# Performance work log

Hardware: AMD Instinct MI355X
Metric: run time of the kernel (lower is better)

Reference implementation:

```python
import jax, jax.numpy as jnp
import numpy as np

N, E = 50000, 800000
D_IN, D_HID, D_OUT = 128, 128, 64


def sage_conv(x, src, dst, w_l, w_r, b, n_nodes):
    # PyG SAGEConv (aggr='mean', root_weight=True):
    #   out = lin_l(mean_{j in N(i)} x_j) + lin_r(x_i)
    msg_sum = jax.ops.segment_sum(x[src], dst, num_segments=n_nodes)  # [N, d]
    cnt = jax.ops.segment_sum(jnp.ones((src.shape[0],), x.dtype), dst,
                              num_segments=n_nodes)                   # [N]
    mean = msg_sum / jnp.maximum(cnt, 1.0)[:, None]
    return mean @ w_l.T + x @ w_r.T + b


def prelu(x, a):
    return jnp.maximum(x, 0) + a * jnp.minimum(x, 0)


def setup_inputs() -> dict:
    key = jax.random.key(0)
    ks = jax.random.split(key, 12)
    def lin(k, o, i):
        s = 1.0 / np.sqrt(i)
        return jax.random.uniform(k, (o, i), jnp.float32, -s, s)
    x = jax.random.normal(ks[0], (N, D_IN), jnp.float32)
    edge_index = jax.random.randint(ks[1], (2, E), 0, N, jnp.int64)
    return {
        "x": x,
        "edge_index": edge_index,
        "w1l": lin(ks[2], D_HID, D_IN),  "w1r": lin(ks[3], D_HID, D_IN),
        "b1": jnp.zeros((D_HID,), jnp.float32),
        "w2l": lin(ks[4], D_HID, D_HID), "w2r": lin(ks[5], D_HID, D_HID),
        "b2": jnp.zeros((D_HID,), jnp.float32),
        "w3l": lin(ks[6], D_OUT, D_HID), "w3r": lin(ks[7], D_OUT, D_HID),
        "b3": jnp.zeros((D_OUT,), jnp.float32),
        "a": jnp.array(0.25, jnp.float32),  # shared PReLU slope
        "wp": lin(ks[8], 1, D_OUT),
        "bp": jnp.zeros((1,), jnp.float32),
    }


def reference(x, edge_index, w1l, w1r, b1, w2l, w2r, b2, w3l, w3r, b3, a, wp, bp):
    src, dst = edge_index[0], edge_index[1]
    n = x.shape[0]
    h = prelu(sage_conv(x, src, dst, w1l, w1r, b1, n), a)
    h = prelu(sage_conv(h, src, dst, w2l, w2r, b2, n), a)
    h = sage_conv(h, src, dst, w3l, w3r, b3, n)          # [N, D_OUT]
    level = (h @ wp.T + bp).squeeze(-1)                  # [N]
    return level
```

## Files before the change

kernel.cpp:

```cpp
#include <hip/hip_runtime.h>
#include <cstdint>
#include <cstddef>

typedef float f32x4 __attribute__((ext_vector_type(4)));
typedef short short8 __attribute__((ext_vector_type(8)));
typedef __bf16 bf16x8 __attribute__((ext_vector_type(8)));

__device__ __forceinline__ void mfma_bf16(f32x4& d, short8 a, short8 b){
  d = __builtin_amdgcn_mfma_f32_16x16x32_bf16(
        __builtin_bit_cast(bf16x8, a), __builtin_bit_cast(bf16x8, b), d, 0, 0, 0);
}

__device__ __forceinline__ unsigned short bf16_rn(float f){
  unsigned u = __float_as_uint(f);
  unsigned r = (u + 0x7FFF + ((u >> 16) & 1)) >> 16;
  return (unsigned short)r;
}

__device__ __forceinline__ int blockScan256Excl(int v, int* wsum){
  const int lane = threadIdx.x & 63, wv = threadIdx.x >> 6;
  int x = v;
  #pragma unroll
  for (int off = 1; off < 64; off <<= 1){
    int y = __shfl_up(x, off);
    if (lane >= off) x += y;
  }
  if (lane == 63) wsum[wv] = x;
  __syncthreads();
  int woff = 0;
  #pragma unroll
  for (int w = 0; w < 4; ++w) woff += (w < wv) ? wsum[w] : 0;
  return woff + x - v;
}

__global__ __launch_bounds__(256) void k_bcount(const int* __restrict__ dst, int E, int nb, int ntiles,
                                                int* __restrict__ blk_hist){
  __shared__ int h[256];
  const int tile = blockIdx.x;
  h[threadIdx.x] = 0;
  __syncthreads();
  const int base = tile * 2048;
  const int end = min(base + 2048, E);
  for (int i = base + threadIdx.x; i < end; i += 256)
    atomicAdd(&h[dst[i] >> 8], 1);
  __syncthreads();
  const int b = threadIdx.x;
  if (b < nb) blk_hist[(size_t)b * ntiles + tile] = h[b];
}

__global__ __launch_bounds__(256) void k_bscan(int* __restrict__ blk_hist, int nb, int ntiles,
                                               int* __restrict__ tot){
  __shared__ int wsum[4];
  __shared__ int carry;
  const int b = blockIdx.x;
  int* row = blk_hist + (size_t)b * ntiles;
  if (threadIdx.x == 0) carry = 0;
  __syncthreads();
  const int lane = threadIdx.x & 63, wv = threadIdx.x >> 6;
  for (int base = 0; base < ntiles; base += 256){
    const int i = base + threadIdx.x;
    const int v = (i < ntiles) ? row[i] : 0;
    int x = v;
    #pragma unroll
    for (int off = 1; off < 64; off <<= 1){
      int y = __shfl_up(x, off);
      if (lane >= off) x += y;
    }
    if (lane == 63) wsum[wv] = x;
    __syncthreads();
    int woff = 0;
    #pragma unroll
    for (int w = 0; w < 4; ++w) woff += (w < wv) ? wsum[w] : 0;
    const int incl = carry + woff + x;
    if (i < ntiles) row[i] = incl - v;
    __syncthreads();
    if (threadIdx.x == 255) carry = incl;
    __syncthreads();
  }
  if (threadIdx.x == 0) tot[b] = carry;
}

__global__ __launch_bounds__(256) void k_btot(const int* __restrict__ tot, int nb,
                                              int* __restrict__ bucket_base){
  __shared__ int wsum[4];
  const int t = threadIdx.x;
  const int v = (t < nb) ? tot[t] : 0;
  const int e = blockScan256Excl(v, wsum);
  if (t <= nb) bucket_base[t] = e;
}

__global__ __launch_bounds__(256) void k_bscat(const int* __restrict__ src, const int* __restrict__ dst,
                                               int E, int nb, int ntiles,
                                               const int* __restrict__ blk_off,
                                               const int* __restrict__ bucket_base,
                                               unsigned* __restrict__ ebuf){
  __shared__ int cnt[256];
  __shared__ int lofs[256];
  __shared__ int gbase[256];
  __shared__ unsigned sorted[2048];
  __shared__ unsigned char sb[2048];
  __shared__ int wsum[4];
  const int tile = blockIdx.x;
  cnt[threadIdx.x] = 0;
  __syncthreads();
  const int base = tile * 2048;
  const int end = min(base + 2048, E);
  const int m = end - base;

  int rank_[8]; int b_[8]; unsigned v_[8];
  #pragma unroll
  for (int k = 0; k < 8; ++k){
    const int j = threadIdx.x + k * 256;
    if (base + j < end){
      const int d = dst[base + j];
      const int s = src[base + j];
      const int b = d >> 8;
      b_[k] = b;
      v_[k] = ((unsigned)(d & 255) << 16) | (unsigned)s;
      rank_[k] = atomicAdd(&cnt[b], 1);
    } else b_[k] = -1;
  }
  __syncthreads();
  const int ex = blockScan256Excl(cnt[threadIdx.x], wsum);
  lofs[threadIdx.x] = ex;
  if (threadIdx.x < nb)
    gbase[threadIdx.x] = bucket_base[threadIdx.x] + blk_off[(size_t)threadIdx.x * ntiles + tile];
  __syncthreads();
  #pragma unroll
  for (int k = 0; k < 8; ++k){
    if (b_[k] >= 0){
      const int p = lofs[b_[k]] + rank_[k];
      sorted[p] = v_[k];
      sb[p] = (unsigned char)b_[k];
    }
  }
  __syncthreads();
  for (int j = threadIdx.x; j < m; j += 256){
    const int b = sb[j];
    ebuf[gbase[b] + (j - lofs[b])] = sorted[j];
  }
}

__global__ __launch_bounds__(256) void k_csrfin(const unsigned* __restrict__ ebuf,
                                                const int* __restrict__ bucket_base,
                                                int n, int E, int nb,
                                                int* __restrict__ row_ptr,
                                                float* __restrict__ inv,
                                                unsigned short* __restrict__ csr){
  __shared__ int hist[256], excl[256], cursor[256];
  __shared__ int wsum[4];
  __shared__ unsigned vals[8192];
  __shared__ unsigned short sorted[8192];
  const int b = blockIdx.x;
  const int ebase = bucket_base[b];
  const int ecnt = bucket_base[b + 1] - ebase;
  const int t = threadIdx.x;
  hist[t] = 0;
  __syncthreads();
  for (int j = t; j < ecnt; j += 256){
    const unsigned v = ebuf[ebase + j];
    vals[j] = v;
    atomicAdd(&hist[v >> 16], 1);
  }
  __syncthreads();
  const int ex = blockScan256Excl(hist[t], wsum);
  excl[t] = ex;
  cursor[t] = ex;
  const int node = b * 256 + t;
  if (node < n){
    row_ptr[node] = ebase + ex;
    const int c = hist[t];
    inv[node] = 1.0f / (float)(c > 0 ? c : 1);
  }
  if (b == nb - 1 && t == 0) row_ptr[n] = E;
  __syncthreads();
  for (int j = t; j < ecnt; j += 256){
    const unsigned v = vals[j];
    const int pos = atomicAdd(&cursor[v >> 16], 1);
    sorted[pos] = (unsigned short)(v & 0xFFFFu);
  }
  __syncthreads();
  for (int j = t; j < ecnt; j += 256)
    csr[ebase + j] = sorted[j];
}

__global__ __launch_bounds__(256) void k_cvt(const float* __restrict__ in,
                                             unsigned short* __restrict__ out, int total){
  const int i = (blockIdx.x * 256 + threadIdx.x) * 4;
  if (i >= total) return;
  const float4 v = *(const float4*)&in[i];
  ushort2 a, b;
  a.x = bf16_rn(v.x); a.y = bf16_rn(v.y);
  b.x = bf16_rn(v.z); b.y = bf16_rn(v.w);
  *(ushort2*)&out[i] = a;
  *(ushort2*)&out[i + 2] = b;
}

__global__ __launch_bounds__(256) void k_aggb(const unsigned short* __restrict__ featb,
                                              const unsigned short* __restrict__ csr,
                                              const int* __restrict__ row_ptr,
                                              const float* __restrict__ inv_cnt,
                                              unsigned short* __restrict__ outb, int n){
  const int lane = threadIdx.x & 63;
  const int node = (blockIdx.x * blockDim.x + threadIdx.x) >> 6;
  if (node >= n) return;
  const int beg = row_ptr[node];
  const int end = row_ptr[node + 1];
  const unsigned* __restrict__ fb = (const unsigned*)featb;

  float ax0=0.f, ay0=0.f, ax1=0.f, ay1=0.f, ax2=0.f, ay2=0.f, ax3=0.f, ay3=0.f;
  float ax4=0.f, ay4=0.f, ax5=0.f, ay5=0.f, ax6=0.f, ay6=0.f, ax7=0.f, ay7=0.f;

  int j = beg;
  for (; j + 8 <= end; j += 8){
    const int s0 = csr[j+0], s1 = csr[j+1], s2 = csr[j+2], s3 = csr[j+3];
    const int s4 = csr[j+4], s5 = csr[j+5], s6 = csr[j+6], s7 = csr[j+7];
    const unsigned u0 = fb[(size_t)s0 * 64 + lane];
    const unsigned u1 = fb[(size_t)s1 * 64 + lane];
    const unsigned u2 = fb[(size_t)s2 * 64 + lane];
    const unsigned u3 = fb[(size_t)s3 * 64 + lane];
    const unsigned u4 = fb[(size_t)s4 * 64 + lane];
    const unsigned u5 = fb[(size_t)s5 * 64 + lane];
    const unsigned u6 = fb[(size_t)s6 * 64 + lane];
    const unsigned u7 = fb[(size_t)s7 * 64 + lane];
    ax0 += __uint_as_float(u0 << 16); ay0 += __uint_as_float(u0 & 0xFFFF0000u);
    ax1 += __uint_as_float(u1 << 16); ay1 += __uint_as_float(u1 & 0xFFFF0000u);
    ax2 += __uint_as_float(u2 << 16); ay2 += __uint_as_float(u2 & 0xFFFF0000u);
    ax3 += __uint_as_float(u3 << 16); ay3 += __uint_as_float(u3 & 0xFFFF0000u);
    ax4 += __uint_as_float(u4 << 16); ay4 += __uint_as_float(u4 & 0xFFFF0000u);
    ax5 += __uint_as_float(u5 << 16); ay5 += __uint_as_float(u5 & 0xFFFF0000u);
    ax6 += __uint_as_float(u6 << 16); ay6 += __uint_as_float(u6 & 0xFFFF0000u);
    ax7 += __uint_as_float(u7 << 16); ay7 += __uint_as_float(u7 & 0xFFFF0000u);
  }
  if (j + 4 <= end){
    const int s0 = csr[j+0], s1 = csr[j+1], s2 = csr[j+2], s3 = csr[j+3];
    const unsigned u0 = fb[(size_t)s0 * 64 + lane];
    const unsigned u1 = fb[(size_t)s1 * 64 + lane];
    const unsigned u2 = fb[(size_t)s2 * 64 + lane];
    const unsigned u3 = fb[(size_t)s3 * 64 + lane];
    ax0 += __uint_as_float(u0 << 16); ay0 += __uint_as_float(u0 & 0xFFFF0000u);
    ax1 += __uint_as_float(u1 << 16); ay1 += __uint_as_float(u1 & 0xFFFF0000u);
    ax2 += __uint_as_float(u2 << 16); ay2 += __uint_as_float(u2 & 0xFFFF0000u);
    ax3 += __uint_as_float(u3 << 16); ay3 += __uint_as_float(u3 & 0xFFFF0000u);
    j += 4;
  }
  for (; j < end; ++j){
    const int s = csr[j];
    const unsigned u = fb[(size_t)s * 64 + lane];
    ax4 += __uint_as_float(u << 16); ay4 += __uint_as_float(u & 0xFFFF0000u);
  }

  const float ic = inv_cnt[node];
  const float ox = (((ax0 + ax1) + (ax2 + ax3)) + ((ax4 + ax5) + (ax6 + ax7))) * ic;
  const float oy = (((ay0 + ay1) + (ay2 + ay3)) + ((ay4 + ay5) + (ay6 + ay7))) * ic;
  const unsigned packed = (unsigned)bf16_rn(ox) | ((unsigned)bf16_rn(oy) << 16);
  ((unsigned*)outb)[(size_t)node * 64 + lane] = packed;
}

__global__ void k_wcs(const float* __restrict__ wl, const float* __restrict__ wr,
                      short* __restrict__ bfr){
  int id = blockIdx.x * 256 + threadIdx.x;
  if (id >= 128 * 256) return;
  int c = id >> 8, k = id & 255;
  float w = (k < 128) ? wl[c * 128 + k] : wr[c * 128 + (k - 128)];
  unsigned short h = bf16_rn(w);
  float hf = __uint_as_float((unsigned)h << 16);
  unsigned short l = bf16_rn(w - hf);
  const int nt = c >> 4, mrow = c & 15;
  const int ks = k >> 5, kgrp = (k >> 3) & 3, j = k & 7;
  const int lane = kgrp * 16 + mrow;
  const size_t fbase = (size_t)((ks * 8 + nt) * 2) * 512 + lane * 8 + j;
  bfr[fbase] = (short)h;
  bfr[fbase + 512] = (short)l;
}

__global__ __launch_bounds__(256) void k_gemm_mfma(const unsigned short* __restrict__ A0b,
                                                   const unsigned short* __restrict__ A1b,
                                                   const short* __restrict__ bfr,
                                                   const float* __restrict__ bias,
                                                   const float* __restrict__ alpha_p,
                                                   float* __restrict__ outf,
                                                   unsigned short* __restrict__ outb16,
                                                   int n){
  __shared__ short aT[2][64 * 128];
  const int t = threadIdx.x;
  const int lane = t & 63;
  const int wv = t >> 6;
  const int nodeBase = blockIdx.x * 64;

  #pragma unroll
  for (int tab = 0; tab < 2; ++tab){
    const unsigned short* __restrict__ src = tab ? A1b : A0b;
    #pragma unroll
    for (int it = 0; it < 4; ++it){
      const int chunk = it * 256 + t;
      const int row = chunk >> 4;
      const int slot = chunk & 15;
      int gr = nodeBase + row; if (gr > n - 1) gr = n - 1;
      const uint4 v = *(const uint4*)&src[(size_t)gr * 128 + slot * 8];
      const int sslot = slot ^ (row & 7);
      *(uint4*)((char*)&aT[tab][0] + row * 256 + sslot * 16) = v;
    }
  }
  __syncthreads();

  const short8* __restrict__ Bf = (const short8*)bfr;
  const int mrow = lane & 15;
  const int kgrp = lane >> 4;
  const int arow = wv * 16 + mrow;

  f32x4 acc[8];
  #pragma unroll
  for (int i = 0; i < 8; ++i) acc[i] = (f32x4){0.f, 0.f, 0.f, 0.f};

  #pragma unroll
  for (int ks = 0; ks < 8; ++ks){
    const int tab = ks >> 2;
    const int slot_r = (ks & 3) * 4 + kgrp;
    const short8 aF = *(const short8*)((const char*)&aT[tab][0] + arow * 256 + (slot_r ^ (arow & 7)) * 16);

    short8 bh[8], bl[8];
    const int fb = ks * 16;
    #pragma unroll
    for (int nt = 0; nt < 8; ++nt){
      bh[nt] = Bf[(size_t)(fb + nt * 2 + 0) * 64 + lane];
      bl[nt] = Bf[(size_t)(fb + nt * 2 + 1) * 64 + lane];
    }
    #pragma unroll
    for (int nt = 0; nt < 8; ++nt){
      mfma_bf16(acc[nt], aF, bh[nt]);
      mfma_bf16(acc[nt], aF, bl[nt]);
    }
  }

  const float alpha = *alpha_p;
  const int nodeQ = nodeBase + wv * 16 + kgrp * 4;
  #pragma unroll
  for (int nt = 0; nt < 8; ++nt){
    const int col = nt * 16 + mrow;
    const float bv = bias[col];
    #pragma unroll
    for (int j = 0; j < 4; ++j){
      const int onode = nodeQ + j;
      if (onode < n){
        float v = acc[nt][j] + bv;
        v = fmaxf(v, 0.f) + alpha * fminf(v, 0.f);
        if (outf)   outf[(size_t)onode * 128 + col] = v;
        if (outb16) outb16[(size_t)onode * 128 + col] = bf16_rn(v);
      }
    }
  }
}

__global__ void k_u(const float* __restrict__ w3l, const float* __restrict__ w3r,
                    const float* __restrict__ b3, const float* __restrict__ wp,
                    const float* __restrict__ bp, float* __restrict__ u){
  int k = threadIdx.x;
  float sl = 0.f, sr = 0.f;
  for (int o = 0; o < 64; ++o){
    float w = wp[o];
    sl = fmaf(w, w3l[o * 128 + k], sl);
    sr = fmaf(w, w3r[o * 128 + k], sr);
  }
  u[k] = sl; u[128 + k] = sr;
  if (k == 0){
    float c = bp[0];
    for (int o = 0; o < 64; ++o) c = fmaf(wp[o], b3[o], c);
    u[256] = c;
  }
}

__global__ __launch_bounds__(256) void k_dot(const float* __restrict__ h,
                                             const float* __restrict__ u,
                                             float* __restrict__ s,
                                             float* __restrict__ partial, int n){
  const int lane = threadIdx.x & 63;
  const int i = blockIdx.x * 4 + (threadIdx.x >> 6);
  if (i >= n) return;
  const float2 hv  = *(const float2*)&h[(size_t)i * 128 + lane * 2];
  const float2 ulv = *(const float2*)&u[lane * 2];
  const float2 urv = *(const float2*)&u[128 + lane * 2];
  float sv = hv.x * ulv.x + hv.y * ulv.y;
  float tv = hv.x * urv.x + hv.y * urv.y;
  #pragma unroll
  for (int off = 32; off > 0; off >>= 1){
    sv += __shfl_down(sv, off);
    tv += __shfl_down(tv, off);
  }
  if (lane == 0){ s[i] = sv; partial[i] = tv + u[256]; }
}

__global__ __launch_bounds__(256) void k_final(const float* __restrict__ s, const float* __restrict__ partial,
                        const unsigned short* __restrict__ csr, const int* __restrict__ row_ptr,
                        const float* __restrict__ inv_cnt, float* __restrict__ out, int n){
  const int t = blockIdx.x * blockDim.x + threadIdx.x;
  const int node = t >> 2;
  const int sub = t & 3;
  if (node >= n) return;
  const int b = row_ptr[node], e = row_ptr[node + 1];
  float a0 = 0.f, a1 = 0.f;
  int j = b + sub;
  for (; j + 4 < e; j += 8){
    a0 += s[csr[j]];
    a1 += s[csr[j + 4]];
  }
  if (j < e) a0 += s[csr[j]];
  float acc = a0 + a1;
  acc += __shfl_down(acc, 1);
  acc += __shfl_down(acc, 2);
  if (sub == 0) out[node] = acc * inv_cnt[node] + partial[node];
}

extern "C" void kernel_launch(void* const* d_in, const int* in_sizes, int n_in,
                              void* d_out, int out_size, void* d_ws, size_t ws_size,
                              hipStream_t stream){
  const float* x   = (const float*)d_in[0];
  const int*   ei  = (const int*)d_in[1];
  const float* w1l = (const float*)d_in[2];
  const float* w1r = (const float*)d_in[3];
  const float* b1  = (const float*)d_in[4];
  const float* w2l = (const float*)d_in[5];
  const float* w2r = (const float*)d_in[6];
  const float* b2  = (const float*)d_in[7];
  const float* w3l = (const float*)d_in[8];
  const float* w3r = (const float*)d_in[9];
  const float* b3  = (const float*)d_in[10];
  const float* ap  = (const float*)d_in[11];
  const float* wp  = (const float*)d_in[12];
  const float* bp  = (const float*)d_in[13];

  const int n = out_size;
  const int E = in_sizes[1] / 2;
  const int* srcI = ei;
  const int* dstI = ei + E;

  const int ntiles = (E + 2047) / 2048;
  const int nb = (n + 255) >> 8;

  char* base = (char*)d_ws;
  size_t off = 0;
  auto take = [&](size_t bytes) -> char* {
    off = (off + 255) & ~(size_t)255;
    char* p = base + off;
    off += bytes;
    return p;
  };
  int*      blk_hist = (int*)   take((size_t)nb * ntiles * 4);
  int*      tot      = (int*)   take((size_t)nb * 4);
  int*      bbase    = (int*)   take(((size_t)nb + 1) * 4);
  unsigned* ebuf     = (unsigned*)take((size_t)E * 4);
  int*      rowp     = (int*)   take(((size_t)n + 1) * 4);
  float*    inv      = (float*) take((size_t)n * 4);
  unsigned short* csr = (unsigned short*)take((size_t)E * 2);
  unsigned short* B1b = (unsigned short*)take((size_t)n * 128 * 2);
  float*    B2   = (float*)take((size_t)n * 128 * 4);
  unsigned short* xb  = (unsigned short*)take((size_t)n * 128 * 2);
  unsigned short* h1b = (unsigned short*)take((size_t)n * 128 * 2);
  float*    sbuf = (float*)take((size_t)n * 4);
  float*    pbuf = (float*)take((size_t)n * 4);
  float*    u    = (float*)take(257 * 4);
  short*    bfr  = (short*)take((size_t)128 * 512 * 2);
  (void)ws_size; (void)n_in;

  k_bcount<<<ntiles, 256, 0, stream>>>(dstI, E, nb, ntiles, blk_hist);
  k_bscan <<<nb,     256, 0, stream>>>(blk_hist, nb, ntiles, tot);
  k_btot  <<<1,      256, 0, stream>>>(tot, nb, bbase);
  k_bscat <<<ntiles, 256, 0, stream>>>(srcI, dstI, E, nb, ntiles, blk_hist, bbase, ebuf);
  k_csrfin<<<nb,     256, 0, stream>>>(ebuf, bbase, n, E, nb, rowp, inv, csr);

  k_cvt<<<(n * 128 / 4 + 255) / 256, 256, 0, stream>>>(x, xb, n * 128);

  const int aggGrid  = (n * 64 + 255) / 256;
  const int gemmGrid = (n + 63) / 64;

  k_aggb     <<<aggGrid, 256, 0, stream>>>(xb, csr, rowp, inv, B1b, n);
  k_wcs      <<<128, 256, 0, stream>>>(w1l, w1r, bfr);
  k_gemm_mfma<<<gemmGrid, 256, 0, stream>>>(B1b, xb, bfr, b1, ap, (float*)nullptr, h1b, n);

  k_aggb     <<<aggGrid, 256, 0, stream>>>(h1b, csr, rowp, inv, B1b, n);
  k_wcs      <<<128, 256, 0, stream>>>(w2l, w2r, bfr);
  k_gemm_mfma<<<gemmGrid, 256, 0, stream>>>(B1b, h1b, bfr, b2, ap, B2, (unsigned short*)nullptr, n);

  k_u    <<<1, 128, 0, stream>>>(w3l, w3r, b3, wp, bp, u);
  k_dot  <<<(n + 3) / 4, 256, 0, stream>>>(B2, u, sbuf, pbuf, n);
  k_final<<<(n * 4 + 255) / 256, 256, 0, stream>>>(sbuf, pbuf, csr, rowp, inv, (float*)d_out, n);
}
```

Before: 178.7 us.

## Slice bf16 features into column tiles for cache-local aggregation and fuse dot into GEMM

Node features are stored in 8 column slices (32 bytes per node per slice), and aggregation runs one slice per block group. Each slice's gather working set then fits in cache, and a wave processes 8 neighbors at once with shuffle reductions. The second GEMM epilogue computes the two dot products with the folded layer-3 vector directly, removing the fp32 hidden buffer and the separate k_dot kernel. The cost is eight passes over the CSR per layer, and the GEMM A-loads now come from the strided sliced layout.

```diff
diff --git a/kernel.cpp b/kernel.cpp
--- a/kernel.cpp
+++ b/kernel.cpp
@@ -185,76 +185,44 @@
 }
 
 __global__ __launch_bounds__(256) void k_cvt(const float* __restrict__ in,
-                                             unsigned short* __restrict__ out, int total){
-  const int i = (blockIdx.x * 256 + threadIdx.x) * 4;
-  if (i >= total) return;
-  const float4 v = *(const float4*)&in[i];
-  ushort2 a, b;
-  a.x = bf16_rn(v.x); a.y = bf16_rn(v.y);
-  b.x = bf16_rn(v.z); b.y = bf16_rn(v.w);
-  *(ushort2*)&out[i] = a;
-  *(ushort2*)&out[i + 2] = b;
-}
-
-__global__ __launch_bounds__(256) void k_aggb(const unsigned short* __restrict__ featb,
+                                             unsigned* __restrict__ slice, int n){
+  const int id = blockIdx.x * 256 + threadIdx.x;
+  if (id >= n * 64) return;
+  const int node = id >> 6, ui = id & 63;
+  const float2 v = *(const float2*)&in[(size_t)id * 2];
+  const unsigned packed = (unsigned)bf16_rn(v.x) | ((unsigned)bf16_rn(v.y) << 16);
+  slice[((size_t)(ui >> 3) * n + node) * 8 + (ui & 7)] = packed;
+}
+
+__global__ __launch_bounds__(256) void k_aggt(const unsigned* __restrict__ slice,
                                               const unsigned short* __restrict__ csr,
                                               const int* __restrict__ row_ptr,
                                               const float* __restrict__ inv_cnt,
-                                              unsigned short* __restrict__ outb, int n){
+                                              unsigned* __restrict__ outb,
+                                              int n){
+  const int bid = blockIdx.x;
+  const int ctile = bid & 7;
+  const int node = (bid >> 3) * 4 + (threadIdx.x >> 6);
+  if (node >= n) return;
   const int lane = threadIdx.x & 63;
-  const int node = (blockIdx.x * blockDim.x + threadIdx.x) >> 6;
-  if (node >= n) return;
-  const int beg = row_ptr[node];
-  const int end = row_ptr[node + 1];
-  const unsigned* __restrict__ fb = (const unsigned*)featb;
-
-  float ax0=0.f, ay0=0.f, ax1=0.f, ay1=0.f, ax2=0.f, ay2=0.f, ax3=0.f, ay3=0.f;
-  float ax4=0.f, ay4=0.f, ax5=0.f, ay5=0.f, ax6=0.f, ay6=0.f, ax7=0.f, ay7=0.f;
-
-  int j = beg;
-  for (; j + 8 <= end; j += 8){
-    const int s0 = csr[j+0], s1 = csr[j+1], s2 = csr[j+2], s3 = csr[j+3];
-    const int s4 = csr[j+4], s5 = csr[j+5], s6 = csr[j+6], s7 = csr[j+7];
-    const unsigned u0 = fb[(size_t)s0 * 64 + lane];
-    const unsigned u1 = fb[(size_t)s1 * 64 + lane];
-    const unsigned u2 = fb[(size_t)s2 * 64 + lane];
-    const unsigned u3 = fb[(size_t)s3 * 64 + lane];
-    const unsigned u4 = fb[(size_t)s4 * 64 + lane];
-    const unsigned u5 = fb[(size_t)s5 * 64 + lane];
-    const unsigned u6 = fb[(size_t)s6 * 64 + lane];
-    const unsigned u7 = fb[(size_t)s7 * 64 + lane];
-    ax0 += __uint_as_float(u0 << 16); ay0 += __uint_as_float(u0 & 0xFFFF0000u);
-    ax1 += __uint_as_float(u1 << 16); ay1 += __uint_as_float(u1 & 0xFFFF0000u);
-    ax2 += __uint_as_float(u2 << 16); ay2 += __uint_as_float(u2 & 0xFFFF0000u);
-    ax3 += __uint_as_float(u3 << 16); ay3 += __uint_as_float(u3 & 0xFFFF0000u);
-    ax4 += __uint_as_float(u4 << 16); ay4 += __uint_as_float(u4 & 0xFFFF0000u);
-    ax5 += __uint_as_float(u5 << 16); ay5 += __uint_as_float(u5 & 0xFFFF0000u);
-    ax6 += __uint_as_float(u6 << 16); ay6 += __uint_as_float(u6 & 0xFFFF0000u);
-    ax7 += __uint_as_float(u7 << 16); ay7 += __uint_as_float(u7 & 0xFFFF0000u);
-  }
-  if (j + 4 <= end){
-    const int s0 = csr[j+0], s1 = csr[j+1], s2 = csr[j+2], s3 = csr[j+3];
-    const unsigned u0 = fb[(size_t)s0 * 64 + lane];
-    const unsigned u1 = fb[(size_t)s1 * 64 + lane];
-    const unsigned u2 = fb[(size_t)s2 * 64 + lane];
-    const unsigned u3 = fb[(size_t)s3 * 64 + lane];
-    ax0 += __uint_as_float(u0 << 16); ay0 += __uint_as_float(u0 & 0xFFFF0000u);
-    ax1 += __uint_as_float(u1 << 16); ay1 += __uint_as_float(u1 & 0xFFFF0000u);
-    ax2 += __uint_as_float(u2 << 16); ay2 += __uint_as_float(u2 & 0xFFFF0000u);
-    ax3 += __uint_as_float(u3 << 16); ay3 += __uint_as_float(u3 & 0xFFFF0000u);
-    j += 4;
-  }
-  for (; j < end; ++j){
-    const int s = csr[j];
-    const unsigned u = fb[(size_t)s * 64 + lane];
-    ax4 += __uint_as_float(u << 16); ay4 += __uint_as_float(u & 0xFFFF0000u);
-  }
-
-  const float ic = inv_cnt[node];
-  const float ox = (((ax0 + ax1) + (ax2 + ax3)) + ((ax4 + ax5) + (ax6 + ax7))) * ic;
-  const float oy = (((ay0 + ay1) + (ay2 + ay3)) + ((ay4 + ay5) + (ay6 + ay7))) * ic;
-  const unsigned packed = (unsigned)bf16_rn(ox) | ((unsigned)bf16_rn(oy) << 16);
-  ((unsigned*)outb)[(size_t)node * 64 + lane] = packed;
+  const int ns = lane >> 3;
+  const int ls = lane & 7;
+  const unsigned* __restrict__ tb = slice + (size_t)ctile * n * 8;
+  const int beg = row_ptr[node], end = row_ptr[node + 1];
+  float ax = 0.f, ay = 0.f;
+  for (int j = beg + ns; j < end; j += 8){
+    const unsigned u = tb[(size_t)csr[j] * 8 + ls];
+    ax += __uint_as_float(u << 16);
+    ay += __uint_as_float(u & 0xFFFF0000u);
+  }
+  ax += __shfl_xor(ax, 8);  ay += __shfl_xor(ay, 8);
+  ax += __shfl_xor(ax, 16); ay += __shfl_xor(ay, 16);
+  ax += __shfl_xor(ax, 32); ay += __shfl_xor(ay, 32);
+  if (lane < 8){
+    const float ic = inv_cnt[node];
+    const unsigned packed = (unsigned)bf16_rn(ax * ic) | ((unsigned)bf16_rn(ay * ic) << 16);
+    outb[(size_t)node * 64 + ctile * 8 + ls] = packed;
+  }
 }
 
 __global__ void k_wcs(const float* __restrict__ wl, const float* __restrict__ wr,
@@ -274,13 +242,15 @@
   bfr[fbase + 512] = (short)l;
 }
 
-__global__ __launch_bounds__(256) void k_gemm_mfma(const unsigned short* __restrict__ A0b,
-                                                   const unsigned short* __restrict__ A1b,
+__global__ __launch_bounds__(256) void k_gemm_mfma(const unsigned* __restrict__ A0u,
+                                                   const unsigned* __restrict__ A1s,
                                                    const short* __restrict__ bfr,
                                                    const float* __restrict__ bias,
                                                    const float* __restrict__ alpha_p,
-                                                   float* __restrict__ outf,
-                                                   unsigned short* __restrict__ outb16,
+                                                   unsigned short* __restrict__ out16s,
+                                                   const float* __restrict__ uvec,
+                                                   float* __restrict__ sbuf,
+                                                   float* __restrict__ pbuf,
                                                    int n){
   __shared__ short aT[2][64 * 128];
   const int t = threadIdx.x;
@@ -290,14 +260,15 @@
 
   #pragma unroll
   for (int tab = 0; tab < 2; ++tab){
-    const unsigned short* __restrict__ src = tab ? A1b : A0b;
     #pragma unroll
     for (int it = 0; it < 4; ++it){
       const int chunk = it * 256 + t;
       const int row = chunk >> 4;
       const int slot = chunk & 15;
       int gr = nodeBase + row; if (gr > n - 1) gr = n - 1;
-      const uint4 v = *(const uint4*)&src[(size_t)gr * 128 + slot * 8];
+      const uint4 v = (tab == 0)
+        ? *(const uint4*)&A0u[(size_t)gr * 64 + slot * 4]
+        : *(const uint4*)&A1s[((size_t)(slot >> 1) * n + gr) * 8 + (slot & 1) * 4];
       const int sslot = slot ^ (row & 7);
       *(uint4*)((char*)&aT[tab][0] + row * 256 + sslot * 16) = v;
     }
@@ -335,18 +306,55 @@
 
   const float alpha = *alpha_p;
   const int nodeQ = nodeBase + wv * 16 + kgrp * 4;
-  #pragma unroll
-  for (int nt = 0; nt < 8; ++nt){
-    const int col = nt * 16 + mrow;
-    const float bv = bias[col];
-    #pragma unroll
-    for (int j = 0; j < 4; ++j){
-      const int onode = nodeQ + j;
-      if (onode < n){
+
+  if (out16s){
+    #pragma unroll
+    for (int nt = 0; nt < 8; ++nt){
+      const int col = nt * 16 + mrow;
+      const float bv = bias[col];
+      #pragma unroll
+      for (int j = 0; j < 4; ++j){
+        const int onode = nodeQ + j;
+        if (onode < n){
+          float v = acc[nt][j] + bv;
+          v = fmaxf(v, 0.f) + alpha * fminf(v, 0.f);
+          out16s[((size_t)nt * n + onode) * 16 + mrow] = bf16_rn(v);
+        }
+      }
+    }
+  } else {
+    float sdot[4] = {0,0,0,0}, tdot[4] = {0,0,0,0};
+    #pragma unroll
+    for (int nt = 0; nt < 8; ++nt){
+      const int col = nt * 16 + mrow;
+      const float bv = bias[col];
+      const float ul = uvec[col];
+      const float ur = uvec[128 + col];
+      #pragma unroll
+      for (int j = 0; j < 4; ++j){
         float v = acc[nt][j] + bv;
         v = fmaxf(v, 0.f) + alpha * fminf(v, 0.f);
-        if (outf)   outf[(size_t)onode * 128 + col] = v;
-        if (outb16) outb16[(size_t)onode * 128 + col] = bf16_rn(v);
+        sdot[j] = fmaf(v, ul, sdot[j]);
+        tdot[j] = fmaf(v, ur, tdot[j]);
+      }
+    }
+    #pragma unroll
+    for (int j = 0; j < 4; ++j){
+      #pragma unroll
+      for (int off = 1; off < 16; off <<= 1){
+        sdot[j] += __shfl_xor(sdot[j], off);
+        tdot[j] += __shfl_xor(tdot[j], off);
+      }
+    }
+    if (mrow == 0){
+      const float c = uvec[256];
+      #pragma unroll
+      for (int j = 0; j < 4; ++j){
+        const int onode = nodeQ + j;
+        if (onode < n){
+          sbuf[onode] = sdot[j];
+          pbuf[onode] = tdot[j] + c;
+        }
       }
     }
   }
@@ -368,26 +376,6 @@
     for (int o = 0; o < 64; ++o) c = fmaf(wp[o], b3[o], c);
     u[256] = c;
   }
-}
-
-__global__ __launch_bounds__(256) void k_dot(const float* __restrict__ h,
-                                             const float* __restrict__ u,
-                                             float* __restrict__ s,
-                                             float* __restrict__ partial, int n){
-  const int lane = threadIdx.x & 63;
-  const int i = blockIdx.x * 4 + (threadIdx.x >> 6);
-  if (i >= n) return;
-  const float2 hv  = *(const float2*)&h[(size_t)i * 128 + lane * 2];
-  const float2 ulv = *(const float2*)&u[lane * 2];
-  const float2 urv = *(const float2*)&u[128 + lane * 2];
-  float sv = hv.x * ulv.x + hv.y * ulv.y;
-  float tv = hv.x * urv.x + hv.y * urv.y;
-  #pragma unroll
-  for (int off = 32; off > 0; off >>= 1){
-    sv += __shfl_down(sv, off);
-    tv += __shfl_down(tv, off);
-  }
-  if (lane == 0){ s[i] = sv; partial[i] = tv + u[256]; }
 }
 
 __global__ __launch_bounds__(256) void k_final(const float* __restrict__ s, const float* __restrict__ partial,
@@ -452,10 +440,9 @@
   int*      rowp     = (int*)   take(((size_t)n + 1) * 4);
   float*    inv      = (float*) take((size_t)n * 4);
   unsigned short* csr = (unsigned short*)take((size_t)E * 2);
-  unsigned short* B1b = (unsigned short*)take((size_t)n * 128 * 2);
-  float*    B2   = (float*)take((size_t)n * 128 * 4);
-  unsigned short* xb  = (unsigned short*)take((size_t)n * 128 * 2);
-  unsigned short* h1b = (unsigned short*)take((size_t)n * 128 * 2);
+  unsigned* B1u = (unsigned*)take((size_t)n * 64 * 4);
+  unsigned* xbs = (unsigned*)take((size_t)n * 64 * 4);
+  unsigned* h1s = (unsigned*)take((size_t)n * 64 * 4);
   float*    sbuf = (float*)take((size_t)n * 4);
   float*    pbuf = (float*)take((size_t)n * 4);
   float*    u    = (float*)take(257 * 4);
@@ -468,20 +455,21 @@
   k_bscat <<<ntiles, 256, 0, stream>>>(srcI, dstI, E, nb, ntiles, blk_hist, bbase, ebuf);
   k_csrfin<<<nb,     256, 0, stream>>>(ebuf, bbase, n, E, nb, rowp, inv, csr);
 
-  k_cvt<<<(n * 128 / 4 + 255) / 256, 256, 0, stream>>>(x, xb, n * 128);
-
-  const int aggGrid  = (n * 64 + 255) / 256;
+  k_cvt<<<(n * 64 + 255) / 256, 256, 0, stream>>>(x, xbs, n);
+
+  const int aggGrid  = ((n + 3) / 4) * 8;
   const int gemmGrid = (n + 63) / 64;
 
-  k_aggb     <<<aggGrid, 256, 0, stream>>>(xb, csr, rowp, inv, B1b, n);
+  k_aggt     <<<aggGrid, 256, 0, stream>>>(xbs, csr, rowp, inv, B1u, n);
   k_wcs      <<<128, 256, 0, stream>>>(w1l, w1r, bfr);
-  k_gemm_mfma<<<gemmGrid, 256, 0, stream>>>(B1b, xb, bfr, b1, ap, (float*)nullptr, h1b, n);
-
-  k_aggb     <<<aggGrid, 256, 0, stream>>>(h1b, csr, rowp, inv, B1b, n);
+  k_gemm_mfma<<<gemmGrid, 256, 0, stream>>>(B1u, xbs, bfr, b1, ap, (unsigned short*)h1s,
+                                            (const float*)nullptr, (float*)nullptr, (float*)nullptr, n);
+
+  k_u        <<<1, 128, 0, stream>>>(w3l, w3r, b3, wp, bp, u);
+  k_aggt     <<<aggGrid, 256, 0, stream>>>(h1s, csr, rowp, inv, B1u, n);
   k_wcs      <<<128, 256, 0, stream>>>(w2l, w2r, bfr);
-  k_gemm_mfma<<<gemmGrid, 256, 0, stream>>>(B1b, h1b, bfr, b2, ap, B2, (unsigned short*)nullptr, n);
-
-  k_u    <<<1, 128, 0, stream>>>(w3l, w3r, b3, wp, bp, u);
-  k_dot  <<<(n + 3) / 4, 256, 0, stream>>>(B2, u, sbuf, pbuf, n);
+  k_gemm_mfma<<<gemmGrid, 256, 0, stream>>>(B1u, h1s, bfr, b2, ap, (unsigned short*)nullptr,
+                                            u, sbuf, pbuf, n);
+
   k_final<<<(n * 4 + 255) / 256, 256, 0, stream>>>(sbuf, pbuf, csr, rowp, inv, (float*)d_out, n);
 }
```

Result: slower. 310.3 us (+73.6%).
